# Kernel optimization log

Hardware: AMD Instinct MI355X
Metric: run time of the kernel (lower is better)

Reference implementation:

```python
import jax, jax.numpy as jnp
import numpy as np

IN_C = 1024
MID = 256
S_C = 256
TOPK_FRAC = 0.25  # atten_topk in (0,1) -> fraction of H*W


def stanh(x):
    return 1.7159 * jnp.tanh(2.0 * x / 3.0)


def setup_inputs() -> dict:
    key = jax.random.key(0)
    ks = jax.random.split(key, 5)
    B, H, W = 32, 28, 28
    x = jax.random.normal(ks[0], (B, IN_C, H, W), jnp.float32)
    s = jax.random.normal(ks[1], (B, S_C), jnp.float32)
    Wq_w = jax.random.normal(ks[2], (MID, IN_C), jnp.float32) * 0.02
    Wq_b = jnp.zeros((MID,), jnp.float32)
    Uq_w = jax.random.normal(ks[3], (MID, S_C), jnp.float32) * 0.02
    w_w = jax.random.normal(ks[4], (IN_C, MID), jnp.float32) * 0.02
    w_b = jnp.zeros((IN_C,), jnp.float32)
    return {"x": x, "s": s, "Wq_w": Wq_w, "Wq_b": Wq_b, "Uq_w": Uq_w, "w_w": w_w, "w_b": w_b}


def reference(x, s, Wq_w, Wq_b, Uq_w, w_w, w_b):
    B, C, H, W = x.shape
    # 1x1 conv Wq(x) + Uq(s) broadcast over spatial, then scaled tanh
    proj = (jnp.einsum('bchw,mc->bmhw', x, Wq_w)
            + Wq_b[None, :, None, None]
            + jnp.einsum('bs,ms->bm', s, Uq_w)[:, :, None, None])
    sig = stanh(proj)  # [B, MID, H, W]
    # 1x1 conv back to in_channel
    alpha = jnp.einsum('bmhw,cm->bchw', sig, w_w) + w_b[None, :, None, None]
    alpha = alpha.reshape(B, C, H * W)
    # topk threshold per (b, c): zero out entries strictly below the k-th largest
    k = int(TOPK_FRAC * H * W)
    th = jax.lax.top_k(alpha, k)[0][..., -1:]  # [B, C, 1]
    alpha = jnp.where(alpha < th, jnp.zeros_like(alpha), alpha)
    # softmax over spatial dim (zeros still contribute exp(0), matching torch)
    atten = jax.nn.softmax(alpha, axis=2)  # [B, C, HW]
    # weighted spatial reduce: c[b,c] = sum_n x[b,c,n] * atten[b,c,n]
    c = jnp.einsum('bcn,bcn->bc', x.reshape(B, C, -1), atten)
    return (c, atten)
```

## Files before the change

### kernel.cpp

```cpp
#include <hip/hip_runtime.h>
#include <hip/hip_bf16.h>
#include <hip/hip_fp16.h>
#include <math.h>

#define BATCH 32
#define INC 1024
#define MIDC 256
#define SC 256
#define HW 784
#define ROWS 25088
#define KSEL 196
#define NV 13

typedef _Float16 f16;
typedef __attribute__((ext_vector_type(8))) _Float16 hfrag;
typedef __attribute__((ext_vector_type(4))) float f4;

struct alignas(8) h4s { f16 x, y, z, w; };

__device__ inline float stanh_fast(float p) {
    float e = __expf(1.33333333f * p);
    return 1.7159f * (1.0f - 2.0f / (e + 1.0f));
}

__global__ __launch_bounds__(256) void cvt_f16(const float* __restrict__ src,
                                               f16* __restrict__ dst, int n4) {
    int i = blockIdx.x * 256 + threadIdx.x;
    if (i >= n4) return;
    float4 v = ((const float4*)src)[i];
    h4s h = { (f16)v.x, (f16)v.y, (f16)v.z, (f16)v.w };
    ((h4s*)dst)[i] = h;
}

__global__ __launch_bounds__(256) void prep_x(const float* __restrict__ x,
                                              f16* __restrict__ xh) {
    int b = blockIdx.z, c0 = blockIdx.y * 32, n0 = blockIdx.x * 32;
    __shared__ float tile[32][33];
    int t = threadIdx.x;
    int r = t >> 3, cg = (t & 7) * 4;
    if (n0 + cg + 3 < HW) {
        float4 v = *(const float4*)(x + (size_t)(b * INC + c0 + r) * HW + n0 + cg);
        tile[r][cg + 0] = v.x; tile[r][cg + 1] = v.y;
        tile[r][cg + 2] = v.z; tile[r][cg + 3] = v.w;
    }
    __syncthreads();
    int rn = t >> 3, cg2 = (t & 7) * 4;
    int n = n0 + rn;
    if (n < HW) {
        h4s h = { (f16)tile[cg2 + 0][rn], (f16)tile[cg2 + 1][rn],
                  (f16)tile[cg2 + 2][rn], (f16)tile[cg2 + 3][rn] };
        *(h4s*)(xh + ((size_t)b * HW + n) * INC + c0 + cg2) = h;
    }
}

__global__ __launch_bounds__(256) void calc_u(const float* __restrict__ s,
                                              const float* __restrict__ Uq_w,
                                              const float* __restrict__ Wq_b,
                                              float* __restrict__ u) {
    __shared__ float ssh[SC];
    int b = blockIdx.x, m = threadIdx.x;
    ssh[m] = s[b * SC + m];
    __syncthreads();
    float acc = Wq_b[m];
    const float* uq = Uq_w + (size_t)m * SC;
    #pragma unroll 8
    for (int i = 0; i < SC; ++i) acc += ssh[i] * uq[i];
    u[b * MIDC + m] = acc;
}

__global__ __launch_bounds__(256) void gemm1_mfma(
    const f16* __restrict__ A,
    const f16* __restrict__ B,
    const float* __restrict__ u,
    f16* __restrict__ S) {
    const int R0 = blockIdx.x * 64;
    const int M0 = blockIdx.y * 128;
    __shared__ f16 Asm[128][40];
    __shared__ f16 Bsm[64][40];
    const int t = threadIdx.x;
    const int lane = t & 63, w = t >> 6;
    const int wc = (w >> 1) * 64;
    const int wr = (w & 1) * 32;
    const int ln = lane & 15, kg = lane >> 4;

    const int ar0 = t >> 2, ar1 = ar0 + 64;
    const int akc = (t & 3) * 8;
    const size_t aoff0 = (size_t)(M0 + ar0) * INC + akc;
    const size_t aoff1 = (size_t)(M0 + ar1) * INC + akc;
    const size_t boff  = (size_t)(R0 + ar0) * INC + akc;

    f4 acc[4][2];
    const f4 zero = {0.f, 0.f, 0.f, 0.f};
    #pragma unroll
    for (int i = 0; i < 4; ++i) { acc[i][0] = zero; acc[i][1] = zero; }

    hfrag rA0, rA1, rB;
    #define G1_LOAD(K0)                                   \
        rA0 = *(const hfrag*)(A + aoff0 + (K0));          \
        rA1 = *(const hfrag*)(A + aoff1 + (K0));          \
        rB  = *(const hfrag*)(B + boff  + (K0));

    G1_LOAD(0)
    for (int k0 = 0; k0 < INC; k0 += 32) {
        *(hfrag*)&Asm[ar0][akc] = rA0;
        *(hfrag*)&Asm[ar1][akc] = rA1;
        *(hfrag*)&Bsm[ar0][akc] = rB;
        __syncthreads();
        if (k0 + 32 < INC) { G1_LOAD(k0 + 32) }
        hfrag b0 = *(const hfrag*)&Bsm[wr + ln][kg * 8];
        hfrag b1 = *(const hfrag*)&Bsm[wr + 16 + ln][kg * 8];
        #pragma unroll
        for (int mi = 0; mi < 4; ++mi) {
            hfrag a = *(const hfrag*)&Asm[wc + mi * 16 + ln][kg * 8];
            acc[mi][0] = __builtin_amdgcn_mfma_f32_16x16x32_f16(a, b0, acc[mi][0], 0, 0, 0);
            acc[mi][1] = __builtin_amdgcn_mfma_f32_16x16x32_f16(a, b1, acc[mi][1], 0, 0, 0);
        }
        __syncthreads();
    }
    #undef G1_LOAD

    #pragma unroll
    for (int ni = 0; ni < 2; ++ni) {
        int R = R0 + wr + ni * 16 + ln;
        int b = R / HW;
        #pragma unroll
        for (int mi = 0; mi < 4; ++mi) {
            int mb = M0 + wc + mi * 16 + kg * 4;
            float uv[4];
            *(float4*)uv = *(const float4*)(u + b * MIDC + mb);
            h4s hv;
            hv.x = (f16)stanh_fast(acc[mi][ni][0] + uv[0]);
            hv.y = (f16)stanh_fast(acc[mi][ni][1] + uv[1]);
            hv.z = (f16)stanh_fast(acc[mi][ni][2] + uv[2]);
            hv.w = (f16)stanh_fast(acc[mi][ni][3] + uv[3]);
            *(h4s*)(S + (size_t)R * MIDC + mb) = hv;
        }
    }
}

__global__ __launch_bounds__(256) void gemm2_mfma(
    const f16* __restrict__ A,
    const f16* __restrict__ B,
    const float* __restrict__ wb,
    float* __restrict__ aout) {
    const int R0 = blockIdx.x * 128;
    const int C0 = blockIdx.y * 128;
    __shared__ f16 Asm[128][40];
    __shared__ f16 Bsm[128][40];
    const int t = threadIdx.x;
    const int lane = t & 63, w = t >> 6;
    const int wc = (w >> 1) * 64;
    const int wr = (w & 1) * 64;
    const int ln = lane & 15, kg = lane >> 4;

    const int r0 = t >> 2, r1 = r0 + 64;
    const int kc = (t & 3) * 8;
    const size_t aoff0 = (size_t)(C0 + r0) * MIDC + kc;
    const size_t aoff1 = (size_t)(C0 + r1) * MIDC + kc;
    const size_t boff0 = (size_t)(R0 + r0) * MIDC + kc;
    const size_t boff1 = (size_t)(R0 + r1) * MIDC + kc;

    f4 acc[4][4];
    const f4 zero = {0.f, 0.f, 0.f, 0.f};
    #pragma unroll
    for (int i = 0; i < 4; ++i)
        #pragma unroll
        for (int j = 0; j < 4; ++j) acc[i][j] = zero;

    hfrag rA0, rA1, rB0, rB1;
    #define G2_LOAD(K0)                                   \
        rA0 = *(const hfrag*)(A + aoff0 + (K0));          \
        rA1 = *(const hfrag*)(A + aoff1 + (K0));          \
        rB0 = *(const hfrag*)(B + boff0 + (K0));          \
        rB1 = *(const hfrag*)(B + boff1 + (K0));

    G2_LOAD(0)
    for (int k0 = 0; k0 < MIDC; k0 += 32) {
        *(hfrag*)&Asm[r0][kc] = rA0;
        *(hfrag*)&Asm[r1][kc] = rA1;
        *(hfrag*)&Bsm[r0][kc] = rB0;
        *(hfrag*)&Bsm[r1][kc] = rB1;
        __syncthreads();
        if (k0 + 32 < MIDC) { G2_LOAD(k0 + 32) }
        hfrag bh[4];
        #pragma unroll
        for (int ni = 0; ni < 4; ++ni)
            bh[ni] = *(const hfrag*)&Bsm[wr + ni * 16 + ln][kg * 8];
        #pragma unroll
        for (int mi = 0; mi < 4; ++mi) {
            hfrag a = *(const hfrag*)&Asm[wc + mi * 16 + ln][kg * 8];
            #pragma unroll
            for (int ni = 0; ni < 4; ++ni)
                acc[mi][ni] = __builtin_amdgcn_mfma_f32_16x16x32_f16(a, bh[ni], acc[mi][ni], 0, 0, 0);
        }
        __syncthreads();
    }
    #undef G2_LOAD

    #pragma unroll
    for (int ni = 0; ni < 4; ++ni) {
        int R = R0 + wr + ni * 16 + ln;
        int b = R / HW;
        int n = R - b * HW;
        float* arow = aout + (size_t)b * INC * HW + n;
        #pragma unroll
        for (int mi = 0; mi < 4; ++mi) {
            int cb = C0 + wc + mi * 16 + kg * 4;
            float wv[4];
            *(float4*)wv = *(const float4*)(wb + cb);
            #pragma unroll
            for (int r = 0; r < 4; ++r)
                arow[(size_t)(cb + r) * HW] = acc[mi][ni][r] + wv[r];
        }
    }
}

__global__ __launch_bounds__(256) void topk_softmax_reduce(const float* __restrict__ x,
                                                           float* __restrict__ out) {
    const int wid  = threadIdx.x >> 6;
    const int lane = threadIdx.x & 63;
    const int row  = blockIdx.x * 4 + wid;
    float* arow = out + BATCH * INC + (size_t)row * HW;
    const float* xrow = x + (size_t)row * HW;

    __shared__ int hist[4][4][264];
    int* hp0 = &hist[wid][0][0];
    const int g = lane >> 4;

    float    v[NV];
    uint32_t key[NV];
    #pragma unroll
    for (int i = 0; i < NV; ++i) {
        int n = lane + 64 * i;
        bool ok = (n < HW);
        float f = ok ? arow[n] : 0.0f;
        v[i] = f;
        uint32_t uu = __float_as_uint(f);
        uint32_t k = (uu & 0x80000000u) ? ~uu : (uu | 0x80000000u);
        key[i] = ok ? k : 0u;
    }

    int kk = KSEL;
    uint32_t prefix = 0;

    {
        const int4 z4 = {0, 0, 0, 0};
        #pragma unroll
        for (int j = 0; j < 5; ++j) {
            int idx = lane + 64 * j;
            if (idx < 264) ((int4*)hp0)[idx] = z4;
        }
        __syncthreads();
        #pragma unroll
        for (int i = 0; i < NV; ++i)
            atomicAdd(&hist[wid][g][key[i] >> 24], 1);
        __syncthreads();
        int4 c0 = *(const int4*)&hist[wid][0][4 * lane];
        int4 c1 = *(const int4*)&hist[wid][1][4 * lane];
        int4 c2 = *(const int4*)&hist[wid][2][4 * lane];
        int4 c3 = *(const int4*)&hist[wid][3][4 * lane];
        int h0 = c0.x + c1.x + c2.x + c3.x;
        int h1 = c0.y + c1.y + c2.y + c3.y;
        int h2 = c0.z + c1.z + c2.z + c3.z;
        int h3 = c0.w + c1.w + c2.w + c3.w;
        int gsum = h0 + h1 + h2 + h3;
        int suf = gsum;
        #pragma unroll
        for (int off = 1; off < 64; off <<= 1) {
            int o = __shfl_down(suf, off, 64);
            suf += (lane + off < 64) ? o : 0;
        }
        int ex = suf - gsum;
        int cgt3 = ex, cgt2 = cgt3 + h3, cgt1 = cgt2 + h2, cgt0 = cgt1 + h1;
        int bsel = -1, cg = 0;
        if (cgt0 < kk && kk <= cgt0 + h0) { bsel = 4 * lane + 0; cg = cgt0; }
        if (cgt1 < kk && kk <= cgt1 + h1) { bsel = 4 * lane + 1; cg = cgt1; }
        if (cgt2 < kk && kk <= cgt2 + h2) { bsel = 4 * lane + 2; cg = cgt2; }
        if (cgt3 < kk && kk <= cgt3 + h3) { bsel = 4 * lane + 3; cg = cgt3; }
        unsigned long long m = __ballot(bsel >= 0);
        int src = (int)__ffsll((long long)m) - 1;
        bsel = __shfl(bsel, src, 64);
        cg   = __shfl(cg,   src, 64);
        kk -= cg;
        prefix = ((uint32_t)bsel) << 24;
        __syncthreads();
    }

    #pragma unroll
    for (int round = 1; round < 4; ++round) {
        const int shift = 24 - 8 * round;
        const uint32_t himask = 0xFFFFFFFFu << (shift + 8);
        const int4 z4 = {0, 0, 0, 0};
        ((int4*)hp0)[lane] = z4;
        __syncthreads();
        #pragma unroll
        for (int i = 0; i < NV; ++i) {
            if ((key[i] & himask) == prefix)
                atomicAdd(&hp0[(key[i] >> shift) & 255], 1);
        }
        __syncthreads();
        int4 c = *(const int4*)&hp0[4 * lane];
        int h0 = c.x, h1 = c.y, h2 = c.z, h3 = c.w;
        int gsum = h0 + h1 + h2 + h3;
        int suf = gsum;
        #pragma unroll
        for (int off = 1; off < 64; off <<= 1) {
            int o = __shfl_down(suf, off, 64);
            suf += (lane + off < 64) ? o : 0;
        }
        int ex = suf - gsum;
        int cgt3 = ex, cgt2 = cgt3 + h3, cgt1 = cgt2 + h2, cgt0 = cgt1 + h1;
        int bsel = -1, cg = 0;
        if (cgt0 < kk && kk <= cgt0 + h0) { bsel = 4 * lane + 0; cg = cgt0; }
        if (cgt1 < kk && kk <= cgt1 + h1) { bsel = 4 * lane + 1; cg = cgt1; }
        if (cgt2 < kk && kk <= cgt2 + h2) { bsel = 4 * lane + 2; cg = cgt2; }
        if (cgt3 < kk && kk <= cgt3 + h3) { bsel = 4 * lane + 3; cg = cgt3; }
        unsigned long long m = __ballot(bsel >= 0);
        int src = (int)__ffsll((long long)m) - 1;
        bsel = __shfl(bsel, src, 64);
        cg   = __shfl(cg,   src, 64);
        kk -= cg;
        prefix |= ((uint32_t)bsel) << shift;
        __syncthreads();
    }

    uint32_t tu = (prefix & 0x80000000u) ? (prefix ^ 0x80000000u) : ~prefix;
    const float th = __uint_as_float(tu);

    float mx = -INFINITY;
    #pragma unroll
    for (int i = 0; i < NV; ++i) {
        int n = lane + 64 * i;
        float f = v[i];
        f = (f < th) ? 0.0f : f;
        v[i] = f;
        if (n < HW) mx = fmaxf(mx, f);
    }
    #pragma unroll
    for (int off = 32; off; off >>= 1) mx = fmaxf(mx, __shfl_xor(mx, off, 64));

    float sum = 0.f;
    #pragma unroll
    for (int i = 0; i < NV; ++i) {
        int n = lane + 64 * i;
        float e = __expf(v[i] - mx);
        v[i] = e;
        if (n < HW) sum += e;
    }
    #pragma unroll
    for (int off = 32; off; off >>= 1) sum += __shfl_xor(sum, off, 64);
    float inv = 1.0f / sum;

    float dot = 0.f;
    #pragma unroll
    for (int i = 0; i < NV; ++i) {
        int n = lane + 64 * i;
        if (n < HW) {
            float a = v[i] * inv;
            arow[n] = a;
            dot += xrow[n] * a;
        }
    }
    #pragma unroll
    for (int off = 32; off; off >>= 1) dot += __shfl_xor(dot, off, 64);
    if (lane == 0) out[row] = dot;
}

extern "C" void kernel_launch(void* const* d_in, const int* in_sizes, int n_in,
                              void* d_out, int out_size, void* d_ws, size_t ws_size,
                              hipStream_t stream) {
    const float* x    = (const float*)d_in[0];
    const float* s    = (const float*)d_in[1];
    const float* Wq_w = (const float*)d_in[2];
    const float* Wq_b = (const float*)d_in[3];
    const float* Uq_w = (const float*)d_in[4];
    const float* w_w  = (const float*)d_in[5];
    const float* w_b  = (const float*)d_in[6];
    float* out = (float*)d_out;

    f16* xt   = (f16*)d_ws;
    f16* sig  = xt + (size_t)ROWS * INC;
    f16* wq_h = sig + (size_t)ROWS * MIDC;
    f16* ww_h = wq_h + MIDC * INC;
    float* u  = (float*)(ww_h + INC * MIDC);
    float* alpha = out + BATCH * INC;

    cvt_f16<<<256, 256, 0, stream>>>(Wq_w, wq_h, MIDC * INC / 4);
    cvt_f16<<<256, 256, 0, stream>>>(w_w, ww_h, INC * MIDC / 4);
    prep_x<<<dim3(25, 32, 32), 256, 0, stream>>>(x, xt);
    calc_u<<<BATCH, 256, 0, stream>>>(s, Uq_w, Wq_b, u);
    gemm1_mfma<<<dim3(ROWS / 64, 2), 256, 0, stream>>>(wq_h, xt, u, sig);
    gemm2_mfma<<<dim3(ROWS / 128, 8), 256, 0, stream>>>(ww_h, sig, w_b, alpha);
    topk_softmax_reduce<<<BATCH * INC / 4, 256, 0, stream>>>(x, out);
}
```

Baseline: 184.3 us.

## Vectorize top-k row I/O, drop block barriers, and exit radix select early

The per-row top-k/softmax kernel now loads and stores each row as float4 chunks instead of scalar strided accesses, and reads x with float4 in the final dot product. The radix-select loop drops its __syncthreads calls, since each wave owns a private histogram. It also stops early when the selected bucket's remaining rank is the bucket's max or min, finding the threshold with a wave-wide max/min reduction. This cuts memory transactions, barrier stalls and later histogram rounds, at the cost of relying on wave-level LDS ordering without explicit barriers and extra per-lane registers (16 values instead of 13).

```diff
diff --git a/kernel.cpp b/kernel.cpp
--- a/kernel.cpp
+++ b/kernel.cpp
@@ -10,7 +10,6 @@
 #define HW 784
 #define ROWS 25088
 #define KSEL 196
-#define NV 13
 
 typedef _Float16 f16;
 typedef __attribute__((ext_vector_type(8))) _Float16 hfrag;
@@ -227,138 +226,158 @@
     int* hp0 = &hist[wid][0][0];
     const int g = lane >> 4;
 
-    float    v[NV];
-    uint32_t key[NV];
-    #pragma unroll
-    for (int i = 0; i < NV; ++i) {
-        int n = lane + 64 * i;
-        bool ok = (n < HW);
-        float f = ok ? arow[n] : 0.0f;
-        v[i] = f;
-        uint32_t uu = __float_as_uint(f);
+    const bool has3 = (lane < 4);
+    float4 v4[4];
+    uint32_t key[16];
+
+    {
+        const float4* ap = (const float4*)arow;
+        v4[0] = ap[lane];
+        v4[1] = ap[lane + 64];
+        v4[2] = ap[lane + 128];
+        v4[3] = has3 ? ap[192 + lane] : make_float4(0.f, 0.f, 0.f, 0.f);
+    }
+    const float* vv = (const float*)v4;
+    #pragma unroll
+    for (int i = 0; i < 16; ++i) {
+        bool ok = (i < 12) | has3;
+        uint32_t uu = __float_as_uint(vv[i]);
         uint32_t k = (uu & 0x80000000u) ? ~uu : (uu | 0x80000000u);
         key[i] = ok ? k : 0u;
     }
 
     int kk = KSEL;
     uint32_t prefix = 0;
-
-    {
-        const int4 z4 = {0, 0, 0, 0};
-        #pragma unroll
-        for (int j = 0; j < 5; ++j) {
-            int idx = lane + 64 * j;
-            if (idx < 264) ((int4*)hp0)[idx] = z4;
-        }
-        __syncthreads();
-        #pragma unroll
-        for (int i = 0; i < NV; ++i)
-            atomicAdd(&hist[wid][g][key[i] >> 24], 1);
-        __syncthreads();
-        int4 c0 = *(const int4*)&hist[wid][0][4 * lane];
-        int4 c1 = *(const int4*)&hist[wid][1][4 * lane];
-        int4 c2 = *(const int4*)&hist[wid][2][4 * lane];
-        int4 c3 = *(const int4*)&hist[wid][3][4 * lane];
-        int h0 = c0.x + c1.x + c2.x + c3.x;
-        int h1 = c0.y + c1.y + c2.y + c3.y;
-        int h2 = c0.z + c1.z + c2.z + c3.z;
-        int h3 = c0.w + c1.w + c2.w + c3.w;
-        int gsum = h0 + h1 + h2 + h3;
-        int suf = gsum;
-        #pragma unroll
-        for (int off = 1; off < 64; off <<= 1) {
-            int o = __shfl_down(suf, off, 64);
-            suf += (lane + off < 64) ? o : 0;
-        }
-        int ex = suf - gsum;
-        int cgt3 = ex, cgt2 = cgt3 + h3, cgt1 = cgt2 + h2, cgt0 = cgt1 + h1;
-        int bsel = -1, cg = 0;
-        if (cgt0 < kk && kk <= cgt0 + h0) { bsel = 4 * lane + 0; cg = cgt0; }
-        if (cgt1 < kk && kk <= cgt1 + h1) { bsel = 4 * lane + 1; cg = cgt1; }
-        if (cgt2 < kk && kk <= cgt2 + h2) { bsel = 4 * lane + 2; cg = cgt2; }
-        if (cgt3 < kk && kk <= cgt3 + h3) { bsel = 4 * lane + 3; cg = cgt3; }
-        unsigned long long m = __ballot(bsel >= 0);
-        int src = (int)__ffsll((long long)m) - 1;
-        bsel = __shfl(bsel, src, 64);
-        cg   = __shfl(cg,   src, 64);
-        kk -= cg;
-        prefix = ((uint32_t)bsel) << 24;
-        __syncthreads();
-    }
-
-    #pragma unroll
-    for (int round = 1; round < 4; ++round) {
-        const int shift = 24 - 8 * round;
-        const uint32_t himask = 0xFFFFFFFFu << (shift + 8);
-        const int4 z4 = {0, 0, 0, 0};
-        ((int4*)hp0)[lane] = z4;
-        __syncthreads();
-        #pragma unroll
-        for (int i = 0; i < NV; ++i) {
-            if ((key[i] & himask) == prefix)
-                atomicAdd(&hp0[(key[i] >> shift) & 255], 1);
-        }
-        __syncthreads();
-        int4 c = *(const int4*)&hp0[4 * lane];
-        int h0 = c.x, h1 = c.y, h2 = c.z, h3 = c.w;
-        int gsum = h0 + h1 + h2 + h3;
-        int suf = gsum;
-        #pragma unroll
-        for (int off = 1; off < 64; off <<= 1) {
-            int o = __shfl_down(suf, off, 64);
-            suf += (lane + off < 64) ? o : 0;
-        }
-        int ex = suf - gsum;
-        int cgt3 = ex, cgt2 = cgt3 + h3, cgt1 = cgt2 + h2, cgt0 = cgt1 + h1;
-        int bsel = -1, cg = 0;
-        if (cgt0 < kk && kk <= cgt0 + h0) { bsel = 4 * lane + 0; cg = cgt0; }
-        if (cgt1 < kk && kk <= cgt1 + h1) { bsel = 4 * lane + 1; cg = cgt1; }
-        if (cgt2 < kk && kk <= cgt2 + h2) { bsel = 4 * lane + 2; cg = cgt2; }
-        if (cgt3 < kk && kk <= cgt3 + h3) { bsel = 4 * lane + 3; cg = cgt3; }
-        unsigned long long m = __ballot(bsel >= 0);
-        int src = (int)__ffsll((long long)m) - 1;
-        bsel = __shfl(bsel, src, 64);
-        cg   = __shfl(cg,   src, 64);
-        kk -= cg;
-        prefix |= ((uint32_t)bsel) << shift;
-        __syncthreads();
-    }
-
-    uint32_t tu = (prefix & 0x80000000u) ? (prefix ^ 0x80000000u) : ~prefix;
+    uint32_t thkey = 0;
+    bool done = false;
+
+    #pragma unroll
+    for (int round = 0; round < 4; ++round) {
+        if (!done) {
+            const int shift = 24 - 8 * round;
+            const int4 z4 = {0, 0, 0, 0};
+            if (round == 0) {
+                #pragma unroll
+                for (int j = 0; j < 5; ++j) {
+                    int idx = lane + 64 * j;
+                    if (idx < 264) ((int4*)hp0)[idx] = z4;
+                }
+                #pragma unroll
+                for (int i = 0; i < 16; ++i)
+                    if (key[i]) atomicAdd(&hist[wid][g][key[i] >> 24], 1);
+            } else {
+                ((int4*)hp0)[lane] = z4;
+                const uint32_t himask = 0xFFFFFFFFu << (shift + 8);
+                #pragma unroll
+                for (int i = 0; i < 16; ++i)
+                    if ((key[i] & himask) == prefix)
+                        atomicAdd(&hp0[(key[i] >> shift) & 255], 1);
+            }
+
+            int h0, h1, h2, h3;
+            if (round == 0) {
+                int4 c0 = *(const int4*)&hist[wid][0][4 * lane];
+                int4 c1 = *(const int4*)&hist[wid][1][4 * lane];
+                int4 c2 = *(const int4*)&hist[wid][2][4 * lane];
+                int4 c3 = *(const int4*)&hist[wid][3][4 * lane];
+                h0 = c0.x + c1.x + c2.x + c3.x;
+                h1 = c0.y + c1.y + c2.y + c3.y;
+                h2 = c0.z + c1.z + c2.z + c3.z;
+                h3 = c0.w + c1.w + c2.w + c3.w;
+            } else {
+                int4 c = *(const int4*)&hp0[4 * lane];
+                h0 = c.x; h1 = c.y; h2 = c.z; h3 = c.w;
+            }
+            int gsum = h0 + h1 + h2 + h3;
+            int suf = gsum;
+            #pragma unroll
+            for (int off = 1; off < 64; off <<= 1) {
+                int o = __shfl_down(suf, off, 64);
+                suf += (lane + off < 64) ? o : 0;
+            }
+            int ex = suf - gsum;
+            int cgt3 = ex, cgt2 = cgt3 + h3, cgt1 = cgt2 + h2, cgt0 = cgt1 + h1;
+            int bsel = -1, cg = 0, hs = 0;
+            if (cgt0 < kk && kk <= cgt0 + h0) { bsel = 4 * lane + 0; cg = cgt0; hs = h0; }
+            if (cgt1 < kk && kk <= cgt1 + h1) { bsel = 4 * lane + 1; cg = cgt1; hs = h1; }
+            if (cgt2 < kk && kk <= cgt2 + h2) { bsel = 4 * lane + 2; cg = cgt2; hs = h2; }
+            if (cgt3 < kk && kk <= cgt3 + h3) { bsel = 4 * lane + 3; cg = cgt3; hs = h3; }
+            unsigned long long m = __ballot(bsel >= 0);
+            int src = (int)__ffsll((long long)m) - 1;
+            bsel = __shfl(bsel, src, 64);
+            cg   = __shfl(cg,   src, 64);
+            hs   = __shfl(hs,   src, 64);
+            kk -= cg;
+            prefix |= ((uint32_t)bsel) << shift;
+
+            if (shift == 0) {
+                thkey = prefix;
+                done = true;
+            } else if (kk == 1 || kk == hs) {
+                const uint32_t maskP = 0xFFFFFFFFu << shift;
+                bool want_max = (kk == 1);
+                uint32_t r = want_max ? 0u : 0xFFFFFFFFu;
+                #pragma unroll
+                for (int i = 0; i < 16; ++i) {
+                    if ((key[i] & maskP) == prefix)
+                        r = want_max ? (r > key[i] ? r : key[i])
+                                     : (r < key[i] ? r : key[i]);
+                }
+                #pragma unroll
+                for (int off = 32; off; off >>= 1) {
+                    uint32_t o = __shfl_xor(r, off, 64);
+                    r = want_max ? (r > o ? r : o) : (r < o ? r : o);
+                }
+                thkey = r;
+                done = true;
+            }
+        }
+    }
+
+    uint32_t tu = (thkey & 0x80000000u) ? (thkey ^ 0x80000000u) : ~thkey;
     const float th = __uint_as_float(tu);
 
+    float* vw = (float*)v4;
     float mx = -INFINITY;
     #pragma unroll
-    for (int i = 0; i < NV; ++i) {
-        int n = lane + 64 * i;
-        float f = v[i];
+    for (int i = 0; i < 16; ++i) {
+        bool ok = (i < 12) | has3;
+        float f = vw[i];
         f = (f < th) ? 0.0f : f;
-        v[i] = f;
-        if (n < HW) mx = fmaxf(mx, f);
+        vw[i] = f;
+        if (ok) mx = fmaxf(mx, f);
     }
     #pragma unroll
     for (int off = 32; off; off >>= 1) mx = fmaxf(mx, __shfl_xor(mx, off, 64));
 
     float sum = 0.f;
     #pragma unroll
-    for (int i = 0; i < NV; ++i) {
-        int n = lane + 64 * i;
-        float e = __expf(v[i] - mx);
-        v[i] = e;
-        if (n < HW) sum += e;
+    for (int i = 0; i < 16; ++i) {
+        bool ok = (i < 12) | has3;
+        float e = __expf(vw[i] - mx);
+        vw[i] = e;
+        sum += ok ? e : 0.f;
     }
     #pragma unroll
     for (int off = 32; off; off >>= 1) sum += __shfl_xor(sum, off, 64);
     float inv = 1.0f / sum;
 
     float dot = 0.f;
-    #pragma unroll
-    for (int i = 0; i < NV; ++i) {
-        int n = lane + 64 * i;
-        if (n < HW) {
-            float a = v[i] * inv;
-            arow[n] = a;
-            dot += xrow[n] * a;
+    {
+        float4* ap = (float4*)arow;
+        const float4* xp = (const float4*)xrow;
+        #pragma unroll
+        for (int ci = 0; ci < 4; ++ci) {
+            if (ci == 3 && !has3) break;
+            int chunk = (ci < 3) ? (lane + 64 * ci) : (192 + lane);
+            float4 a;
+            a.x = vw[ci * 4 + 0] * inv;
+            a.y = vw[ci * 4 + 1] * inv;
+            a.z = vw[ci * 4 + 2] * inv;
+            a.w = vw[ci * 4 + 3] * inv;
+            ap[chunk] = a;
+            float4 xl = xp[chunk];
+            dot += xl.x * a.x + xl.y * a.y + xl.z * a.z + xl.w * a.w;
         }
     }
     #pragma unroll
```

Result: faster. 179.4 us (-2.7%).
